# Performance work log

Hardware: AMD Instinct MI355X
Metric: run time of the kernel (lower is better)

## Reference

```python
import jax, jax.numpy as jnp
import numpy as np

NUM_HEADS = 6

def setup_inputs() -> dict:
    key = jax.random.key(0)
    k1, k2, k3, k4 = jax.random.split(key, 4)
    B, T, C = 128, 256, 384
    s = 1.0 / np.sqrt(C)
    return {
        'x': jax.random.normal(k1, (B, T, C), dtype=jnp.float32),
        'Wq': jax.random.normal(k2, (C, C), dtype=jnp.float32) * s,
        'Wk': jax.random.normal(k3, (C, C), dtype=jnp.float32) * s,
        'Wv': jax.random.normal(k4, (C, C), dtype=jnp.float32) * s,
    }

def reference(x, Wq, Wk, Wv):
    B, T, C = x.shape
    H = NUM_HEADS
    d = C // H
    # projections (bias-free Linear), split into heads
    q = (x @ Wq).reshape(B, T, H, d)
    k = (x @ Wk).reshape(B, T, H, d)
    v = (x @ Wv).reshape(B, T, H, d)
    # NOTE: original scales by 1/sqrt(C), not 1/sqrt(head_dim)
    scale = 1.0 / jnp.sqrt(jnp.asarray(C, dtype=x.dtype))
    att = jnp.einsum('bqhd,bkhd->bhqk', q, k) * scale  # [B,H,T,T]
    causal = jnp.tril(jnp.ones((T, T), dtype=bool))
    att = jnp.where(causal, att, -jnp.inf)
    att = jax.nn.softmax(att, axis=-1)
    # dropout is identity in eval/deterministic mode
    out = jnp.einsum('bhqk,bkhd->bqhd', att, v)  # [B,T,H,d]
    return out.reshape(B, T, C)
```

## Files before the change

### kernel.cpp

```cpp
#include <hip/hip_runtime.h>


typedef unsigned short u16;
typedef float f32x4 __attribute__((ext_vector_type(4)));
typedef short s16x8 __attribute__((ext_vector_type(8)));

static constexpr int BB = 128;
static constexpr int TT = 256;
static constexpr int CC = 384;
static constexpr int HH = 6;
static constexpr int DD = 64;
static constexpr int MM = BB * TT;

static constexpr size_t QOFF  = 0;
static constexpr size_t KOFF  = (size_t)MM * CC;
static constexpr size_t VOFF  = (size_t)2 * MM * CC;
static constexpr size_t WTOFF = (size_t)3 * MM * CC;
static constexpr size_t XOFF  = WTOFF + (size_t)3 * CC * CC;

static constexpr float CSC = 0.07362242194579907f;

__device__ __forceinline__ u16 f2bf(float f) {
  unsigned u = __float_as_uint(f);
  u += 0x7fffu + ((u >> 16) & 1u);
  return (u16)(u >> 16);
}

__device__ __forceinline__ void g2l16(const u16* g, u16* l) {
  __builtin_amdgcn_global_load_lds(
      (const __attribute__((address_space(1))) u16*)g,
      (__attribute__((address_space(3))) u16*)l, 16, 0, 0);
}

__global__ void prep(const float* __restrict__ X, const float* __restrict__ Wq,
                     const float* __restrict__ Wk, const float* __restrict__ Wv,
                     u16* __restrict__ ws) {
  int bx = blockIdx.x;
  if (bx < 6144) {
    size_t i = (size_t)(bx * 256 + threadIdx.x) * 8;
    f32x4 a0 = *(const f32x4*)(X + i);
    f32x4 a1 = *(const f32x4*)(X + i + 4);
    s16x8 ab;
#pragma unroll
    for (int j = 0; j < 4; ++j) { ab[j] = (short)f2bf(a0[j]); ab[4 + j] = (short)f2bf(a1[j]); }
    *(s16x8*)(ws + XOFF + i) = ab;
  } else {
    int j = bx - 6144;
    int z = j / 576;
    const float* W = (z == 0) ? Wq : (z == 1) ? Wk : Wv;
    const float sc = (z == 0) ? CSC : 1.0f;
    u16* WT = ws + WTOFF + (size_t)z * CC * CC;
    int i = (j % 576) * 256 + threadIdx.x;
    int k = i / CC, n = i % CC;
    WT[(size_t)n * CC + k] = f2bf(W[i] * sc);
  }
}

__global__ __launch_bounds__(256) void gemm_qkv(u16* __restrict__ ws) {
  const u16* Xbf = ws + XOFF;
  const u16* WT3 = ws + WTOFF;

  __shared__ u16 As[128][64];
  __shared__ u16 Bs[128][64];

  const int tid = threadIdx.x;
  const int lane = tid & 63;
  const int w = tid >> 6;
  const int quad = lane >> 4;
  const int col = lane & 15;
  const int m0 = blockIdx.x * 128;
  const int n0 = blockIdx.y * 128;
  const int z = blockIdx.y / 3;
  const int wm = (w >> 1) * 64;
  const int wn = (w & 1) * 64;

  const int rl = lane >> 3;
  const int gb = (lane & 7) ^ rl;

  f32x4 acc[4][4] = {};

  for (int kt = 0; kt < 6; ++kt) {
    if (kt) __syncthreads();
#pragma unroll
    for (int i = 0; i < 4; ++i) {
      int r0 = (w * 4 + i) * 8;
      g2l16(Xbf + (size_t)(m0 + r0 + rl) * CC + kt * 64 + gb * 8, &As[r0][0]);
      g2l16(WT3 + (size_t)(n0 + r0 + rl) * CC + kt * 64 + gb * 8, &Bs[r0][0]);
    }
    __syncthreads();

    s16x8 af[4][2], bf[4][2];
#pragma unroll
    for (int mt = 0; mt < 4; ++mt)
#pragma unroll
      for (int ks = 0; ks < 2; ++ks)
        af[mt][ks] = *(const s16x8*)(&As[wm + mt * 16 + col]
                                        [(((ks * 4 + quad) ^ (col & 7)) * 8)]);
#pragma unroll
    for (int nt = 0; nt < 4; ++nt)
#pragma unroll
      for (int ks = 0; ks < 2; ++ks)
        bf[nt][ks] = *(const s16x8*)(&Bs[wn + nt * 16 + col]
                                        [(((ks * 4 + quad) ^ (col & 7)) * 8)]);

#pragma unroll
    for (int ks = 0; ks < 2; ++ks)
#pragma unroll
      for (int mt = 0; mt < 4; ++mt)
#pragma unroll
        for (int nt = 0; nt < 4; ++nt)
          acc[mt][nt] = __builtin_amdgcn_mfma_f32_16x16x32_bf16(
              af[mt][ks], bf[nt][ks], acc[mt][nt], 0, 0, 0);
  }

  if (z == 2) {
#pragma unroll
    for (int mt = 0; mt < 4; ++mt)
#pragma unroll
      for (int nt = 0; nt < 4; ++nt) {
        int tok = m0 + wm + mt * 16 + quad * 4;
        int bb = tok >> 8, t = tok & 255;
        int ng = (n0 - 2 * CC) + wn + nt * 16 + col;
        int hh = ng >> 6, d = ng & 63;
        uint2 pk;
        pk.x = (unsigned)f2bf(acc[mt][nt][0]) | ((unsigned)f2bf(acc[mt][nt][1]) << 16);
        pk.y = (unsigned)f2bf(acc[mt][nt][2]) | ((unsigned)f2bf(acc[mt][nt][3]) << 16);
        *(uint2*)(ws + VOFF + (((size_t)(bb * HH + hh) * DD + d) * TT + t)) = pk;
      }
  } else {
    u16* Y = ws + (size_t)z * MM * CC;
    const int nz = n0 - z * CC;
#pragma unroll
    for (int mt = 0; mt < 4; ++mt)
#pragma unroll
      for (int nt = 0; nt < 4; ++nt) {
        int mg = m0 + wm + mt * 16 + quad * 4;
        int ng = nz + wn + nt * 16 + col;
#pragma unroll
        for (int r = 0; r < 4; ++r)
          Y[(size_t)(mg + r) * CC + ng] = f2bf(acc[mt][nt][r]);
      }
  }
}

__global__ __launch_bounds__(128) void attn(const u16* __restrict__ ws,
                                            float* __restrict__ out) {
  const int bx = blockIdx.x;
  const int qt = 3 - (bx / 768);
  const int bh = bx % 768;
  const int b = bh / HH;
  const int h = bh % HH;

  __shared__ u16 Ps[2][16][72];

  const int tid = threadIdx.x;
  const int lane = tid & 63;
  const int w = tid >> 6;
  const int quad = lane >> 4;
  const int col = lane & 15;
  const int q0 = qt * 64 + w * 32;

  const u16* Qg = ws + QOFF;
  const u16* Kg = ws + KOFF;
  const u16* VTg = ws + VOFF;

  s16x8 qf[2][2];
#pragma unroll
  for (int mt = 0; mt < 2; ++mt)
#pragma unroll
    for (int ks = 0; ks < 2; ++ks)
      qf[mt][ks] = *(const s16x8*)(Qg + (size_t)(b * TT + q0 + mt * 16 + col) * CC +
                                   h * DD + ks * 32 + quad * 8);

  f32x4 o[2][4] = {};
  float mst[2] = {-1.0e30f, -1.0e30f}, lst[2] = {0.0f, 0.0f};

  for (int kt = 0; kt <= qt; ++kt) {
    s16x8 kf[4][2], vf[4][2];
#pragma unroll
    for (int nt = 0; nt < 4; ++nt)
#pragma unroll
      for (int ks = 0; ks < 2; ++ks) {
        kf[nt][ks] = *(const s16x8*)(Kg + (size_t)(b * TT + kt * 64 + nt * 16 + col) * CC +
                                     h * DD + ks * 32 + quad * 8);
        vf[nt][ks] = *(const s16x8*)(VTg + ((size_t)(bh * DD + nt * 16 + col) * TT +
                                     kt * 64 + ks * 32 + quad * 8));
      }

#pragma unroll
    for (int mt = 0; mt < 2; ++mt) {
      f32x4 s[4] = {};
#pragma unroll
      for (int ks = 0; ks < 2; ++ks)
#pragma unroll
        for (int nt = 0; nt < 4; ++nt)
          s[nt] = __builtin_amdgcn_mfma_f32_16x16x32_bf16(kf[nt][ks], qf[mt][ks],
                                                          s[nt], 0, 0, 0);

      float rmax = -1.0e30f;
#pragma unroll
      for (int nt = 0; nt < 4; ++nt)
#pragma unroll
        for (int r = 0; r < 4; ++r) {
          float t = s[nt][r];
          if (kt == qt && (nt * 16 + quad * 4 + r) > (w * 32 + mt * 16 + col)) t = -1.0e30f;
          s[nt][r] = t;
          rmax = fmaxf(rmax, t);
        }
      rmax = fmaxf(rmax, __shfl_xor(rmax, 16));
      rmax = fmaxf(rmax, __shfl_xor(rmax, 32));

      float mn = fmaxf(mst[mt], rmax);
      float alpha = exp2f(mst[mt] - mn);
      mst[mt] = mn;

      float lsum = 0.0f;
      unsigned pk[4][2];
#pragma unroll
      for (int nt = 0; nt < 4; ++nt) {
        float p0 = exp2f(s[nt][0] - mn), p1 = exp2f(s[nt][1] - mn);
        float p2 = exp2f(s[nt][2] - mn), p3 = exp2f(s[nt][3] - mn);
        lsum += (p0 + p1) + (p2 + p3);
        pk[nt][0] = (unsigned)f2bf(p0) | ((unsigned)f2bf(p1) << 16);
        pk[nt][1] = (unsigned)f2bf(p2) | ((unsigned)f2bf(p3) << 16);
      }
      lst[mt] = lst[mt] * alpha + lsum;

#pragma unroll
      for (int dt = 0; dt < 4; ++dt)
#pragma unroll
        for (int r = 0; r < 4; ++r) o[mt][dt][r] *= alpha;

      asm volatile("s_waitcnt lgkmcnt(0)" ::: "memory");
#pragma unroll
      for (int nt = 0; nt < 4; ++nt)
        *(uint2*)(&Ps[w][col][nt * 16 + quad * 4]) = make_uint2(pk[nt][0], pk[nt][1]);
      asm volatile("s_waitcnt lgkmcnt(0)" ::: "memory");

      s16x8 pf[2];
#pragma unroll
      for (int ks = 0; ks < 2; ++ks)
        pf[ks] = *(const s16x8*)(&Ps[w][col][ks * 32 + quad * 8]);

#pragma unroll
      for (int ks = 0; ks < 2; ++ks)
#pragma unroll
        for (int dt = 0; dt < 4; ++dt)
          o[mt][dt] = __builtin_amdgcn_mfma_f32_16x16x32_bf16(vf[dt][ks], pf[ks],
                                                              o[mt][dt], 0, 0, 0);
    }
  }

#pragma unroll
  for (int mt = 0; mt < 2; ++mt) {
    float l = lst[mt];
    l += __shfl_xor(l, 16);
    l += __shfl_xor(l, 32);
    float inv = 1.0f / l;
    int q = q0 + mt * 16 + col;
#pragma unroll
    for (int dt = 0; dt < 4; ++dt) {
      f32x4 res;
#pragma unroll
      for (int r = 0; r < 4; ++r) res[r] = o[mt][dt][r] * inv;
      *(f32x4*)(out + (size_t)(b * TT + q) * CC + h * DD + dt * 16 + quad * 4) = res;
    }
  }
}

extern "C" void kernel_launch(void* const* d_in, const int* in_sizes, int n_in,
                              void* d_out, int out_size, void* d_ws, size_t ws_size,
                              hipStream_t stream) {
  const float* x  = (const float*)d_in[0];
  const float* wq = (const float*)d_in[1];
  const float* wk = (const float*)d_in[2];
  const float* wv = (const float*)d_in[3];
  u16* ws  = (u16*)d_ws;
  float* out = (float*)d_out;

  prep<<<dim3(6144 + 1728), 256, 0, stream>>>(x, wq, wk, wv, ws);
  gemm_qkv<<<dim3(MM / 128, 9), 256, 0, stream>>>(ws);
  attn<<<dim3(BB * HH * 4), 128, 0, stream>>>(ws, out);
}
```

Baseline: 177.4 us.

## Fuse QKV projection and causal attention into one per-(batch,head) kernel

Replaces the separate QKV GEMM and attention kernels with one kernel per (batch, head). Each block projects its head's Q, K and V from X tiles into shared memory with swizzled layouts, then runs flash-style causal attention straight from LDS. The aim is to drop the global write and re-read of Q/K/V and one kernel launch. Each block recomputes the X load per head, runs only 768 large blocks with heavy LDS use, and pairs query groups (w, 15-w) to balance causal work across warps.

Result: faster. 159.6 us (-10.0%).

```diff
diff --git a/kernel.cpp b/kernel.cpp
--- a/kernel.cpp
+++ b/kernel.cpp
@@ -12,11 +12,8 @@
 static constexpr int DD = 64;
 static constexpr int MM = BB * TT;
 
-static constexpr size_t QOFF  = 0;
-static constexpr size_t KOFF  = (size_t)MM * CC;
-static constexpr size_t VOFF  = (size_t)2 * MM * CC;
-static constexpr size_t WTOFF = (size_t)3 * MM * CC;
-static constexpr size_t XOFF  = WTOFF + (size_t)3 * CC * CC;
+static constexpr size_t WTOFF = 0;
+static constexpr size_t XOFF  = (size_t)3 * CC * CC;
 
 static constexpr float CSC = 0.07362242194579907f;
 
@@ -56,163 +53,164 @@
   }
 }
 
-__global__ __launch_bounds__(256) void gemm_qkv(u16* __restrict__ ws) {
-  const u16* Xbf = ws + XOFF;
-  const u16* WT3 = ws + WTOFF;
-
-  __shared__ u16 As[128][64];
-  __shared__ u16 Bs[128][64];
+__global__ __launch_bounds__(512, 2) void fused(const u16* __restrict__ ws,
+                                                float* __restrict__ out) {
+  const int bid = blockIdx.x;
+  const int xc = bid & 7;
+  const int g5 = bid >> 3;
+  const int b = xc * 16 + g5 / 6;
+  const int h = g5 % 6;
+
+  __shared__ u16 Xs[256][64];
+  __shared__ u16 Ws[192][64];
+  __shared__ u16 Ks[256][64];
+  __shared__ u16 VTs[64][256];
 
   const int tid = threadIdx.x;
   const int lane = tid & 63;
   const int w = tid >> 6;
   const int quad = lane >> 4;
   const int col = lane & 15;
-  const int m0 = blockIdx.x * 128;
-  const int n0 = blockIdx.y * 128;
-  const int z = blockIdx.y / 3;
-  const int wm = (w >> 1) * 64;
-  const int wn = (w & 1) * 64;
+
+  const u16* Xg = ws + XOFF + (size_t)b * TT * CC;
+  const u16* Wg = ws + WTOFF;
 
   const int rl = lane >> 3;
   const int gb = (lane & 7) ^ rl;
 
-  f32x4 acc[4][4] = {};
+  const int wm = (w >> 1) * 64;
+  const int wn = (w & 1) * 96;
+
+  f32x4 acc[4][6] = {};
 
   for (int kt = 0; kt < 6; ++kt) {
     if (kt) __syncthreads();
 #pragma unroll
     for (int i = 0; i < 4; ++i) {
-      int r0 = (w * 4 + i) * 8;
-      g2l16(Xbf + (size_t)(m0 + r0 + rl) * CC + kt * 64 + gb * 8, &As[r0][0]);
-      g2l16(WT3 + (size_t)(n0 + r0 + rl) * CC + kt * 64 + gb * 8, &Bs[r0][0]);
+      int r0 = w * 32 + i * 8;
+      g2l16(Xg + (size_t)(r0 + rl) * CC + kt * 64 + gb * 8, &Xs[r0][0]);
+    }
+#pragma unroll
+    for (int i = 0; i < 3; ++i) {
+      int r0 = w * 24 + i * 8;
+      int rr = r0 + rl;
+      int z = rr >> 6, nn = rr & 63;
+      g2l16(Wg + (size_t)(z * CC + h * DD + nn) * CC + kt * 64 + gb * 8, &Ws[r0][0]);
     }
     __syncthreads();
 
-    s16x8 af[4][2], bf[4][2];
+    s16x8 af[4][2];
 #pragma unroll
     for (int mt = 0; mt < 4; ++mt)
 #pragma unroll
       for (int ks = 0; ks < 2; ++ks)
-        af[mt][ks] = *(const s16x8*)(&As[wm + mt * 16 + col]
+        af[mt][ks] = *(const s16x8*)(&Xs[wm + mt * 16 + col]
                                         [(((ks * 4 + quad) ^ (col & 7)) * 8)]);
 #pragma unroll
-    for (int nt = 0; nt < 4; ++nt)
-#pragma unroll
-      for (int ks = 0; ks < 2; ++ks)
-        bf[nt][ks] = *(const s16x8*)(&Bs[wn + nt * 16 + col]
-                                        [(((ks * 4 + quad) ^ (col & 7)) * 8)]);
-
-#pragma unroll
-    for (int ks = 0; ks < 2; ++ks)
-#pragma unroll
-      for (int mt = 0; mt < 4; ++mt)
-#pragma unroll
-        for (int nt = 0; nt < 4; ++nt)
+    for (int nt = 0; nt < 6; ++nt) {
+      s16x8 bf[2];
+#pragma unroll
+      for (int ks = 0; ks < 2; ++ks)
+        bf[ks] = *(const s16x8*)(&Ws[wn + nt * 16 + col]
+                                    [(((ks * 4 + quad) ^ (col & 7)) * 8)]);
+#pragma unroll
+      for (int ks = 0; ks < 2; ++ks)
+#pragma unroll
+        for (int mt = 0; mt < 4; ++mt)
           acc[mt][nt] = __builtin_amdgcn_mfma_f32_16x16x32_bf16(
-              af[mt][ks], bf[nt][ks], acc[mt][nt], 0, 0, 0);
-  }
-
-  if (z == 2) {
-#pragma unroll
-    for (int mt = 0; mt < 4; ++mt)
-#pragma unroll
-      for (int nt = 0; nt < 4; ++nt) {
-        int tok = m0 + wm + mt * 16 + quad * 4;
-        int bb = tok >> 8, t = tok & 255;
-        int ng = (n0 - 2 * CC) + wn + nt * 16 + col;
-        int hh = ng >> 6, d = ng & 63;
+              af[mt][ks], bf[ks], acc[mt][nt], 0, 0, 0);
+    }
+  }
+  __syncthreads();
+
+#pragma unroll
+  for (int mt = 0; mt < 4; ++mt) {
+    int tokb = wm + mt * 16 + quad * 4;
+#pragma unroll
+    for (int nt = 0; nt < 6; ++nt) {
+      int gn = wn + nt * 16 + col;
+      if (gn < 128) {
+        u16* dst = (gn < 64) ? (u16*)Xs : (u16*)Ks;
+        int d = gn & 63;
+#pragma unroll
+        for (int r = 0; r < 4; ++r) {
+          int tok = tokb + r;
+          dst[tok * 64 + (d ^ ((tok & 7) << 3))] = f2bf(acc[mt][nt][r]);
+        }
+      } else {
+        int d = gn - 128;
         uint2 pk;
         pk.x = (unsigned)f2bf(acc[mt][nt][0]) | ((unsigned)f2bf(acc[mt][nt][1]) << 16);
         pk.y = (unsigned)f2bf(acc[mt][nt][2]) | ((unsigned)f2bf(acc[mt][nt][3]) << 16);
-        *(uint2*)(ws + VOFF + (((size_t)(bb * HH + hh) * DD + d) * TT + t)) = pk;
+        *(uint2*)((u16*)VTs + d * 256 + (tokb ^ ((d & 15) << 3))) = pk;
       }
-  } else {
-    u16* Y = ws + (size_t)z * MM * CC;
-    const int nz = n0 - z * CC;
-#pragma unroll
-    for (int mt = 0; mt < 4; ++mt)
-#pragma unroll
-      for (int nt = 0; nt < 4; ++nt) {
-        int mg = m0 + wm + mt * 16 + quad * 4;
-        int ng = nz + wn + nt * 16 + col;
-#pragma unroll
-        for (int r = 0; r < 4; ++r)
-          Y[(size_t)(mg + r) * CC + ng] = f2bf(acc[mt][nt][r]);
-      }
-  }
-}
-
-__global__ __launch_bounds__(128) void attn(const u16* __restrict__ ws,
-                                            float* __restrict__ out) {
-  const int bx = blockIdx.x;
-  const int qt = 3 - (bx / 768);
-  const int bh = bx % 768;
-  const int b = bh / HH;
-  const int h = bh % HH;
-
-  __shared__ u16 Ps[2][16][72];
-
-  const int tid = threadIdx.x;
-  const int lane = tid & 63;
-  const int w = tid >> 6;
-  const int quad = lane >> 4;
-  const int col = lane & 15;
-  const int q0 = qt * 64 + w * 32;
-
-  const u16* Qg = ws + QOFF;
-  const u16* Kg = ws + KOFF;
-  const u16* VTg = ws + VOFF;
+    }
+  }
+  __syncthreads();
+
+  u16* Ps = (u16*)Ws + (size_t)w * 1152 + (size_t)col * 72;
 
   s16x8 qf[2][2];
 #pragma unroll
-  for (int mt = 0; mt < 2; ++mt)
+  for (int gi = 0; gi < 2; ++gi) {
+    int g = gi ? (15 - w) : w;
+    int q = g * 16 + col;
 #pragma unroll
     for (int ks = 0; ks < 2; ++ks)
-      qf[mt][ks] = *(const s16x8*)(Qg + (size_t)(b * TT + q0 + mt * 16 + col) * CC +
-                                   h * DD + ks * 32 + quad * 8);
+      qf[gi][ks] = *(const s16x8*)((u16*)Xs + q * 64 +
+                                   (((ks * 4 + quad) ^ (q & 7)) << 3));
+  }
 
   f32x4 o[2][4] = {};
   float mst[2] = {-1.0e30f, -1.0e30f}, lst[2] = {0.0f, 0.0f};
 
-  for (int kt = 0; kt <= qt; ++kt) {
+  const int kthi = (15 - w) >> 2;
+  for (int kt = 0; kt <= kthi; ++kt) {
     s16x8 kf[4][2], vf[4][2];
 #pragma unroll
     for (int nt = 0; nt < 4; ++nt)
 #pragma unroll
       for (int ks = 0; ks < 2; ++ks) {
-        kf[nt][ks] = *(const s16x8*)(Kg + (size_t)(b * TT + kt * 64 + nt * 16 + col) * CC +
-                                     h * DD + ks * 32 + quad * 8);
-        vf[nt][ks] = *(const s16x8*)(VTg + ((size_t)(bh * DD + nt * 16 + col) * TT +
-                                     kt * 64 + ks * 32 + quad * 8));
+        int key = kt * 64 + nt * 16 + col;
+        kf[nt][ks] = *(const s16x8*)((u16*)Ks + key * 64 +
+                                     (((ks * 4 + quad) ^ (key & 7)) << 3));
+        int d = nt * 16 + col;
+        vf[nt][ks] = *(const s16x8*)((u16*)VTs + d * 256 +
+                                     ((kt * 64 + ks * 32 + quad * 8) ^ ((d & 15) << 3)));
       }
 
 #pragma unroll
-    for (int mt = 0; mt < 2; ++mt) {
+    for (int gi = 0; gi < 2; ++gi) {
+      const int g = gi ? (15 - w) : w;
+      const int gmax = g >> 2;
+      if (kt > gmax) continue;
+
       f32x4 s[4] = {};
 #pragma unroll
       for (int ks = 0; ks < 2; ++ks)
 #pragma unroll
         for (int nt = 0; nt < 4; ++nt)
-          s[nt] = __builtin_amdgcn_mfma_f32_16x16x32_bf16(kf[nt][ks], qf[mt][ks],
+          s[nt] = __builtin_amdgcn_mfma_f32_16x16x32_bf16(kf[nt][ks], qf[gi][ks],
                                                           s[nt], 0, 0, 0);
 
+      const int qq = (g & 3) * 16 + col;
+      const bool diag = (kt == gmax);
       float rmax = -1.0e30f;
 #pragma unroll
       for (int nt = 0; nt < 4; ++nt)
 #pragma unroll
         for (int r = 0; r < 4; ++r) {
           float t = s[nt][r];
-          if (kt == qt && (nt * 16 + quad * 4 + r) > (w * 32 + mt * 16 + col)) t = -1.0e30f;
+          if (diag && (nt * 16 + quad * 4 + r) > qq) t = -1.0e30f;
           s[nt][r] = t;
           rmax = fmaxf(rmax, t);
         }
       rmax = fmaxf(rmax, __shfl_xor(rmax, 16));
       rmax = fmaxf(rmax, __shfl_xor(rmax, 32));
 
-      float mn = fmaxf(mst[mt], rmax);
-      float alpha = exp2f(mst[mt] - mn);
-      mst[mt] = mn;
+      float mn = fmaxf(mst[gi], rmax);
+      float alpha = exp2f(mst[gi] - mn);
+      mst[gi] = mn;
 
       float lsum = 0.0f;
       unsigned pk[4][2];
@@ -224,45 +222,46 @@
         pk[nt][0] = (unsigned)f2bf(p0) | ((unsigned)f2bf(p1) << 16);
         pk[nt][1] = (unsigned)f2bf(p2) | ((unsigned)f2bf(p3) << 16);
       }
-      lst[mt] = lst[mt] * alpha + lsum;
+      lst[gi] = lst[gi] * alpha + lsum;
 
 #pragma unroll
       for (int dt = 0; dt < 4; ++dt)
 #pragma unroll
-        for (int r = 0; r < 4; ++r) o[mt][dt][r] *= alpha;
+        for (int r = 0; r < 4; ++r) o[gi][dt][r] *= alpha;
 
       asm volatile("s_waitcnt lgkmcnt(0)" ::: "memory");
 #pragma unroll
       for (int nt = 0; nt < 4; ++nt)
-        *(uint2*)(&Ps[w][col][nt * 16 + quad * 4]) = make_uint2(pk[nt][0], pk[nt][1]);
+        *(uint2*)(Ps + nt * 16 + quad * 4) = make_uint2(pk[nt][0], pk[nt][1]);
       asm volatile("s_waitcnt lgkmcnt(0)" ::: "memory");
 
       s16x8 pf[2];
 #pragma unroll
       for (int ks = 0; ks < 2; ++ks)
-        pf[ks] = *(const s16x8*)(&Ps[w][col][ks * 32 + quad * 8]);
+        pf[ks] = *(const s16x8*)(Ps + ks * 32 + quad * 8);
 
 #pragma unroll
       for (int ks = 0; ks < 2; ++ks)
 #pragma unroll
         for (int dt = 0; dt < 4; ++dt)
-          o[mt][dt] = __builtin_amdgcn_mfma_f32_16x16x32_bf16(vf[dt][ks], pf[ks],
-                                                              o[mt][dt], 0, 0, 0);
-    }
-  }
-
-#pragma unroll
-  for (int mt = 0; mt < 2; ++mt) {
-    float l = lst[mt];
+          o[gi][dt] = __builtin_amdgcn_mfma_f32_16x16x32_bf16(vf[dt][ks], pf[ks],
+                                                              o[gi][dt], 0, 0, 0);
+    }
+  }
+
+#pragma unroll
+  for (int gi = 0; gi < 2; ++gi) {
+    int g = gi ? (15 - w) : w;
+    float l = lst[gi];
     l += __shfl_xor(l, 16);
     l += __shfl_xor(l, 32);
     float inv = 1.0f / l;
-    int q = q0 + mt * 16 + col;
+    int q = g * 16 + col;
 #pragma unroll
     for (int dt = 0; dt < 4; ++dt) {
       f32x4 res;
 #pragma unroll
-      for (int r = 0; r < 4; ++r) res[r] = o[mt][dt][r] * inv;
+      for (int r = 0; r < 4; ++r) res[r] = o[gi][dt][r] * inv;
       *(f32x4*)(out + (size_t)(b * TT + q) * CC + h * DD + dt * 16 + quad * 4) = res;
     }
   }
@@ -279,6 +278,5 @@
   float* out = (float*)d_out;
 
   prep<<<dim3(6144 + 1728), 256, 0, stream>>>(x, wq, wk, wv, ws);
-  gemm_qkv<<<dim3(MM / 128, 9), 256, 0, stream>>>(ws);
-  attn<<<dim3(BB * HH * 4), 128, 0, stream>>>(ws, out);
-}
+  fused<<<dim3(BB * HH), 512, 0, stream>>>(ws, out);
+}
```
